# Kernel optimization log

Hardware: AMD Instinct MI355X
Metric: run time of the kernel (lower is better)

Reference implementation:

```python
import jax, jax.numpy as jnp
import numpy as np

N = 50000      # nodes
E = 800000     # edges (avg degree 16)
B = 250        # graphs in batch
T = 8          # temporal slices
CIN = 32
COUT = 64


def setup_inputs() -> dict:
    key = jax.random.key(0)
    ks = jax.random.split(key, 9)
    x = jax.random.normal(ks[0], (N, CIN, T), dtype=jnp.float32)
    edge_index = jax.random.randint(ks[1], (2, E), 0, N, dtype=jnp.int64)
    # 250 graphs of 200 nodes each -> every segment non-empty (safe for segment_max)
    batch = jnp.repeat(jnp.arange(B, dtype=jnp.int64), N // B)
    W1 = jax.random.normal(ks[2], (CIN, COUT), jnp.float32) / np.sqrt(CIN).astype(np.float32)
    b1 = jax.random.normal(ks[3], (COUT,), jnp.float32) * 0.01
    W2 = jax.random.normal(ks[4], (COUT, COUT), jnp.float32) / np.sqrt(COUT).astype(np.float32)
    b2 = jax.random.normal(ks[5], (COUT,), jnp.float32) * 0.01
    W3 = jax.random.normal(ks[6], (COUT, COUT), jnp.float32) / np.sqrt(COUT).astype(np.float32)
    b3 = jax.random.normal(ks[7], (COUT,), jnp.float32) * 0.01
    return {"x": x, "edge_index": edge_index, "batch": batch,
            "W1": W1, "b1": b1, "W2": W2, "b2": b2, "W3": W3, "b3": b3}


def reference(x, edge_index, batch, W1, b1, W2, b2, W3, b3):
    # GCNConv (PyG default): add self-loops, symmetric D^{-1/2}(A+I)D^{-1/2} norm,
    # linear transform then gather-scale-scatter aggregation, plus bias.
    src, dst = edge_index[0], edge_index[1]
    loops = jnp.arange(N, dtype=src.dtype)
    src2 = jnp.concatenate([src, loops])
    dst2 = jnp.concatenate([dst, loops])
    deg = jax.ops.segment_sum(jnp.ones_like(src2, x.dtype), dst2, num_segments=N)
    dinv = jax.lax.rsqrt(deg)  # deg >= 1 due to self-loops
    norm = dinv[src2] * dinv[dst2]  # [E+N]
    counts = jax.ops.segment_sum(jnp.ones((N,), x.dtype), batch, num_segments=B)

    def gcn(h, W, b):
        h = h @ W                              # [N, COUT]
        msg = norm[:, None] * h[src2]          # [E+N, COUT] gather + scale
        return jax.ops.segment_sum(msg, dst2, num_segments=N) + b

    def pool(h):  # cat(global_max_pool, global_mean_pool) -> [B, 2*COUT]
        mx = jax.ops.segment_max(h, batch, num_segments=B)
        mn = jax.ops.segment_sum(h, batch, num_segments=B) / counts[:, None]
        return jnp.concatenate([mx, mn], axis=1)

    def step(carry, xt):  # xt: [N, CIN]
        h1 = jax.nn.relu(gcn(xt, W1, b1))
        h2 = jax.nn.relu(gcn(h1, W2, b2))
        h3 = jax.nn.relu(gcn(h2, W3, b3))
        return carry, pool(h1) + pool(h2) + pool(h3)

    _, outs = jax.lax.scan(step, None, jnp.moveaxis(x, 2, 0))  # [T, B, 2*COUT]
    return jnp.moveaxis(outs, 0, 2)  # [B, 2*COUT, T]
```

## Files before the change

kernel.cpp:

```cpp
#include <hip/hip_runtime.h>
#include <hip/hip_fp16.h>
#include <math.h>

#define NN 50000
#define EE 800000
#define BB 250
#define TT 8
#define CIN 32
#define COUT 64
#define NPG 200
#define SCAN_B 256
#define NBLK 196
#define GC (BB * COUT)

__device__ __forceinline__ float unpack_w(unsigned int v) {
    union { unsigned short u; __half h; } cv;
    cv.u = (unsigned short)(v >> 16);
    return __half2float(cv.h);
}


__global__ void init_deg(int* deg, int* cursor) {
    int n = blockIdx.x * 256 + threadIdx.x;
    if (n < NN) { deg[n] = 1; cursor[n] = 0; }
}

__global__ void count_deg(const int* dst, int* deg) {
    int e = blockIdx.x * 256 + threadIdx.x;
    if (e < EE) atomicAdd(&deg[dst[e]], 1);
}

__global__ void compute_dinv(const int* deg, float* dinv) {
    int n = blockIdx.x * 256 + threadIdx.x;
    if (n < NN) dinv[n] = rsqrtf((float)deg[n]);
}

__global__ void scan_blocks(const int* deg, int* off, int* bsum) {
    __shared__ int sh[SCAN_B];
    int gid = blockIdx.x * SCAN_B + threadIdx.x;
    int v = (gid < NN) ? (deg[gid] - 1) : 0;
    sh[threadIdx.x] = v;
    __syncthreads();
    for (int s = 1; s < SCAN_B; s <<= 1) {
        int add = (threadIdx.x >= s) ? sh[threadIdx.x - s] : 0;
        __syncthreads();
        sh[threadIdx.x] += add;
        __syncthreads();
    }
    if (gid < NN) off[gid] = sh[threadIdx.x] - v;
    if (threadIdx.x == SCAN_B - 1) bsum[blockIdx.x] = sh[threadIdx.x];
}

__global__ void scan_sums(int* bsum, int* off) {
    __shared__ int sh[SCAN_B];
    int v = (threadIdx.x < NBLK) ? bsum[threadIdx.x] : 0;
    sh[threadIdx.x] = v;
    __syncthreads();
    for (int s = 1; s < SCAN_B; s <<= 1) {
        int add = (threadIdx.x >= s) ? sh[threadIdx.x - s] : 0;
        __syncthreads();
        sh[threadIdx.x] += add;
        __syncthreads();
    }
    if (threadIdx.x < NBLK) bsum[threadIdx.x] = sh[threadIdx.x] - v;
    if (threadIdx.x == 0) off[NN] = EE;
}

__global__ void scan_add(int* off, const int* bsum) {
    int gid = blockIdx.x * SCAN_B + threadIdx.x;
    if (gid < NN) off[gid] += bsum[blockIdx.x];
}

__global__ void fill_csr(const int* src, const int* dst, const int* off,
                         int* cursor, const float* dinv, unsigned int* csrp) {
    int e = blockIdx.x * 256 + threadIdx.x;
    if (e >= EE) return;
    int s = src[e], d = dst[e];
    int p = atomicAdd(&cursor[d], 1);
    union { __half h; unsigned short u; } cv;
    cv.h = __float2half(dinv[s] * dinv[d]);
    csrp[off[d] + p] = (unsigned int)s | ((unsigned int)cv.u << 16);
}

__global__ void scratch_init(float* scr, int ntot) {
    int i = blockIdx.x * 256 + threadIdx.x;
    if (i < ntot) scr[i] = 0.f;
}


__global__ void agg_x_allT16(const float* __restrict__ x, const int* __restrict__ off,
                             const unsigned int* __restrict__ csrp,
                             const float* __restrict__ dinv, __half2* __restrict__ xa2) {
    int lane = threadIdx.x & 63;
    int w = threadIdx.x >> 6;
    int n = blockIdx.x * 4 + w;
    float dn = dinv[n];
    float sw = dn * dn;
    float4 v = ((const float4*)(x + (size_t)n * 256))[lane];
    float4 acc = make_float4(sw * v.x, sw * v.y, sw * v.z, sw * v.w);
    int e0 = off[n], e1 = off[n + 1];
    for (int base = e0; base < e1; base += 64) {
        int idx = base + lane;
        unsigned int cme = (idx < e1) ? csrp[idx] : 0u;
        int cnt = min(64, e1 - base);
        int k = 0;
        for (; k + 3 < cnt; k += 4) {
            unsigned int p0 = __shfl(cme, k, 64),     p1 = __shfl(cme, k + 1, 64);
            unsigned int p2 = __shfl(cme, k + 2, 64), p3 = __shfl(cme, k + 3, 64);
            float4 u0 = ((const float4*)(x + (size_t)(p0 & 0xffff) * 256))[lane];
            float4 u1 = ((const float4*)(x + (size_t)(p1 & 0xffff) * 256))[lane];
            float4 u2 = ((const float4*)(x + (size_t)(p2 & 0xffff) * 256))[lane];
            float4 u3 = ((const float4*)(x + (size_t)(p3 & 0xffff) * 256))[lane];
            float w0 = unpack_w(p0), w1 = unpack_w(p1);
            float w2 = unpack_w(p2), w3 = unpack_w(p3);
            acc.x = fmaf(w0, u0.x, acc.x); acc.y = fmaf(w0, u0.y, acc.y);
            acc.z = fmaf(w0, u0.z, acc.z); acc.w = fmaf(w0, u0.w, acc.w);
            acc.x = fmaf(w1, u1.x, acc.x); acc.y = fmaf(w1, u1.y, acc.y);
            acc.z = fmaf(w1, u1.z, acc.z); acc.w = fmaf(w1, u1.w, acc.w);
            acc.x = fmaf(w2, u2.x, acc.x); acc.y = fmaf(w2, u2.y, acc.y);
            acc.z = fmaf(w2, u2.z, acc.z); acc.w = fmaf(w2, u2.w, acc.w);
            acc.x = fmaf(w3, u3.x, acc.x); acc.y = fmaf(w3, u3.y, acc.y);
            acc.z = fmaf(w3, u3.z, acc.z); acc.w = fmaf(w3, u3.w, acc.w);
        }
        for (; k < cnt; ++k) {
            unsigned int p = __shfl(cme, k, 64);
            float wj = unpack_w(p);
            float4 u = ((const float4*)(x + (size_t)(p & 0xffff) * 256))[lane];
            acc.x = fmaf(wj, u.x, acc.x); acc.y = fmaf(wj, u.y, acc.y);
            acc.z = fmaf(wj, u.z, acc.z); acc.w = fmaf(wj, u.w, acc.w);
        }
    }
    __shared__ float sh[4][TT][33];
    float av[4] = {acc.x, acc.y, acc.z, acc.w};
    #pragma unroll
    for (int k = 0; k < 4; ++k) {
        int f = 4 * lane + k;
        sh[w][f & 7][f >> 3] = av[k];
    }
    __syncthreads();
    for (int i = threadIdx.x; i < 512; i += 256) {
        int t = i >> 6;
        int r = i & 63;
        int nl = r >> 4;
        int pp = r & 15;
        xa2[((size_t)(t >> 1) * NN + blockIdx.x * 4 + nl) * 32 + (t & 1) * 16 + pp] =
            __floats2half2_rn(sh[nl][t][2 * pp], sh[nl][t][2 * pp + 1]);
    }
}

__global__ void l1mat2i(const __half2* __restrict__ xa, const float* __restrict__ W1,
                        const float* __restrict__ b1, const float* __restrict__ W2,
                        __half2* __restrict__ H1,
                        float* __restrict__ pmax, float* __restrict__ psum) {
    __shared__ float W1s[CIN * COUT];
    __shared__ __half2 W2s[COUT * 32];
    __shared__ float Xs[4][2][CIN];
    __shared__ float tile[4][2][COUT];
    for (int i = threadIdx.x; i < CIN * COUT; i += 256) W1s[i] = W1[i];
    for (int i = threadIdx.x; i < COUT * 32; i += 256) {
        int k = i >> 5, pr = i & 31;
        W2s[i] = __floats2half2_rn(W2[k * COUT + 2 * pr], W2[k * COUT + 2 * pr + 1]);
    }
    if (threadIdx.x < 128) {
        int nl = threadIdx.x >> 5, idx = threadIdx.x & 31;
        int tc = idx >> 4, pp = idx & 15;
        float2 v = __half22float2(xa[((size_t)blockIdx.x * 4 + nl) * 32 + idx]);
        Xs[nl][tc][2 * pp] = v.x;
        Xs[nl][tc][2 * pp + 1] = v.y;
    }
    __syncthreads();
    int co = threadIdx.x & 63;
    int nl = threadIdx.x >> 6;
    float a0 = b1[co], a1 = b1[co];
    #pragma unroll
    for (int k = 0; k < CIN; ++k) {
        float wv = W1s[k * COUT + co];
        a0 = fmaf(Xs[nl][0][k], wv, a0);
        a1 = fmaf(Xs[nl][1][k], wv, a1);
    }
    tile[nl][0][co] = fmaxf(a0, 0.f);
    tile[nl][1][co] = fmaxf(a1, 0.f);
    __syncthreads();
    if (threadIdx.x < 128) {
        int c = threadIdx.x & 63, tc = threadIdx.x >> 6;
        float m = fmaxf(fmaxf(tile[0][tc][c], tile[1][tc][c]),
                        fmaxf(tile[2][tc][c], tile[3][tc][c]));
        float s = tile[0][tc][c] + tile[1][tc][c] + tile[2][tc][c] + tile[3][tc][c];
        int g = blockIdx.x / 50;
        atomicMax((int*)&pmax[tc * GC + g * COUT + c], __float_as_int(m));
        atomicAdd(&psum[tc * GC + g * COUT + c], s);
    }
    {
        int row = threadIdx.x >> 5;
        int pr = threadIdx.x & 31;
        int nl2 = row >> 1, tc2 = row & 1;
        float b0 = 0.f, bb1 = 0.f;
        #pragma unroll
        for (int k = 0; k < COUT; ++k) {
            float xv = tile[nl2][tc2][k];
            float2 wv = __half22float2(W2s[k * 32 + pr]);
            b0 = fmaf(xv, wv.x, b0);
            bb1 = fmaf(xv, wv.y, bb1);
        }
        H1[((size_t)blockIdx.x * 4 + nl2) * 64 + tc2 * 32 + pr] =
            __floats2half2_rn(b0, bb1);
    }
}

template <int FUSE>
__global__ void agg2q(const __half2* __restrict__ Hin, const int* __restrict__ off,
                      const unsigned int* __restrict__ csrp,
                      const float* __restrict__ dinv, const float* __restrict__ b,
                      const float* __restrict__ W, __half2* __restrict__ Hout,
                      float* __restrict__ pmax, float* __restrict__ psum) {
    __shared__ __half2 Ws[FUSE ? COUT * 32 : 1];
    __shared__ float tile[4][2][COUT];
    if (FUSE)
        for (int i = threadIdx.x; i < COUT * 32; i += 256) {
            int k = i >> 5, pr = i & 31;
            Ws[i] = __floats2half2_rn(W[k * COUT + 2 * pr], W[k * COUT + 2 * pr + 1]);
        }
    int lane = threadIdx.x & 63;
    int w = threadIdx.x >> 6;
    int n = blockIdx.x * 4 + w;
    int e0 = off[n], e1 = off[n + 1];
    float dn = dinv[n];
    __half2 selfh = Hin[(size_t)n * 64 + lane];
    float accx = 0.f, accy = 0.f;

#define QUAD(K)                                                       \
    {                                                                 \
        unsigned int ce0 = __shfl(cme, (K),     64);                  \
        unsigned int ce1 = __shfl(cme, (K) + 1, 64);                  \
        unsigned int ce2 = __shfl(cme, (K) + 2, 64);                  \
        unsigned int ce3 = __shfl(cme, (K) + 3, 64);                  \
        __half2 u0 = Hin[(size_t)(ce0 & 0xffff) * 64 + lane];         \
        __half2 u1 = Hin[(size_t)(ce1 & 0xffff) * 64 + lane];         \
        __half2 u2 = Hin[(size_t)(ce2 & 0xffff) * 64 + lane];         \
        __half2 u3 = Hin[(size_t)(ce3 & 0xffff) * 64 + lane];         \
        float w0 = unpack_w(ce0), w1 = unpack_w(ce1);                 \
        float w2 = unpack_w(ce2), w3 = unpack_w(ce3);                 \
        float2 f0 = __half22float2(u0);                               \
        float2 f1 = __half22float2(u1);                               \
        float2 f2 = __half22float2(u2);                               \
        float2 f3 = __half22float2(u3);                               \
        accx = fmaf(w0, f0.x, accx); accy = fmaf(w0, f0.y, accy);     \
        accx = fmaf(w1, f1.x, accx); accy = fmaf(w1, f1.y, accy);     \
        accx = fmaf(w2, f2.x, accx); accy = fmaf(w2, f2.y, accy);     \
        accx = fmaf(w3, f3.x, accx); accy = fmaf(w3, f3.y, accy);     \
    }

    for (int base = e0; base < e1; base += 64) {
        int idx = base + lane;
        unsigned int cme = (idx < e1) ? csrp[idx] : 0u;
        int cnt = min(64, e1 - base);
        QUAD(0)
        QUAD(4)
        QUAD(8)
        QUAD(12)
        for (int k = 16; k < cnt; k += 4) QUAD(k)
    }
#undef QUAD

    {
        int tc = lane >> 5, p = lane & 31;
        float sw = dn * dn;
        float2 sv = __half22float2(selfh);
        float ox = fmaxf(fmaf(sw, sv.x, accx) + b[2 * p],     0.f);
        float oy = fmaxf(fmaf(sw, sv.y, accy) + b[2 * p + 1], 0.f);
        tile[w][tc][2 * p]     = ox;
        tile[w][tc][2 * p + 1] = oy;
    }
    __syncthreads();
    if (threadIdx.x < 128) {
        int c = threadIdx.x & 63, tcc = threadIdx.x >> 6;
        float m = fmaxf(fmaxf(tile[0][tcc][c], tile[1][tcc][c]),
                        fmaxf(tile[2][tcc][c], tile[3][tcc][c]));
        float s = tile[0][tcc][c] + tile[1][tcc][c] + tile[2][tcc][c] + tile[3][tcc][c];
        int g = blockIdx.x / 50;
        atomicMax((int*)&pmax[tcc * GC + g * COUT + c], __float_as_int(m));
        atomicAdd(&psum[tcc * GC + g * COUT + c], s);
    }
    if (FUSE) {
        int row = threadIdx.x >> 5;
        int pr = threadIdx.x & 31;
        int nl2 = row >> 1, tc2 = row & 1;
        float b0 = 0.f, bb1 = 0.f;
        #pragma unroll
        for (int k = 0; k < COUT; ++k) {
            float xv = tile[nl2][tc2][k];
            float2 wv = __half22float2(Ws[k * 32 + pr]);
            b0 = fmaf(xv, wv.x, b0);
            bb1 = fmaf(xv, wv.y, bb1);
        }
        Hout[((size_t)blockIdx.x * 4 + nl2) * 64 + tc2 * 32 + pr] =
            __floats2half2_rn(b0, bb1);
    }
}

__global__ void fold2(float* __restrict__ pmaxT, float* __restrict__ psumT,
                      float* __restrict__ out, int t0) {
    int i = blockIdx.x * 256 + threadIdx.x;
    if (i >= 2 * GC) return;
    int tc = i / GC;
    int r = i - tc * GC;
    int g = r >> 6, c = r & 63;
    float m = pmaxT[tc * GC + r] + pmaxT[2 * GC + tc * GC + r] +
              pmaxT[4 * GC + tc * GC + r];
    float mean = psumT[i] * (1.0f / NPG);
    int t = t0 + tc;
    out[((size_t)g * 128 + c) * TT + t] = m;
    out[((size_t)g * 128 + 64 + c) * TT + t] = mean;
    pmaxT[tc * GC + r] = 0.f;
    pmaxT[2 * GC + tc * GC + r] = 0.f;
    pmaxT[4 * GC + tc * GC + r] = 0.f;
    psumT[i] = 0.f;
}


extern "C" void kernel_launch(void* const* d_in, const int* in_sizes, int n_in,
                              void* d_out, int out_size, void* d_ws, size_t ws_size,
                              hipStream_t stream) {
    const float* x   = (const float*)d_in[0];
    const int*   ei  = (const int*)d_in[1];
    const int*   src = ei;
    const int*   dst = ei + EE;
    const float* W1  = (const float*)d_in[3];
    const float* b1  = (const float*)d_in[4];
    const float* W2  = (const float*)d_in[5];
    const float* b2  = (const float*)d_in[6];
    const float* W3  = (const float*)d_in[7];
    const float* b3  = (const float*)d_in[8];
    float* out = (float*)d_out;

    char* wsp = (char*)d_ws;
    auto alloc = [&](size_t bytes) {
        char* p = wsp;
        wsp += (bytes + 255) & ~(size_t)255;
        return p;
    };
    const size_t chunkHalf2 = (size_t)NN * 32;
    float*        dinv = (float*)       alloc((size_t)NN * 4);
    int*          off  = (int*)         alloc((size_t)(NN + 1) * 4);
    unsigned int* csrp = (unsigned int*)alloc((size_t)EE * 4);
    __half2*      H1   = (__half2*)     alloc((size_t)NN * 64 * 4);
    __half2*      xa2  = (__half2*)     alloc(chunkHalf2 * 4 * 4);
    __half2*      h2x  = (__half2*)     alloc(chunkHalf2 * 4);
    float*        scr  = (float*)       alloc((size_t)8 * GC * 4);
    (void)h2x;
    __half2* H2 = xa2 + 3 * chunkHalf2;
    float* pmaxT = scr;
    float* psumT = scr + 6 * GC;

    int* deg    = (int*)H1;
    int* cursor = ((int*)H1) + NN;
    int* bsum   = ((int*)H1) + 2 * NN;

    init_deg<<<NBLK, 256, 0, stream>>>(deg, cursor);
    count_deg<<<(EE + 255) / 256, 256, 0, stream>>>(dst, deg);
    compute_dinv<<<NBLK, 256, 0, stream>>>(deg, dinv);
    scan_blocks<<<NBLK, SCAN_B, 0, stream>>>(deg, off, bsum);
    scan_sums<<<1, SCAN_B, 0, stream>>>(bsum, off);
    scan_add<<<NBLK, SCAN_B, 0, stream>>>(off, bsum);
    fill_csr<<<(EE + 255) / 256, 256, 0, stream>>>(src, dst, off, cursor, dinv, csrp);
    scratch_init<<<(8 * GC + 255) / 256, 256, 0, stream>>>(scr, 8 * GC);

    agg_x_allT16<<<NN / 4, 256, 0, stream>>>(x, off, csrp, dinv, xa2);

    for (int c = 3; c >= 0; --c) {
        int t0 = 2 * c;
        const __half2* xc = xa2 + (size_t)c * chunkHalf2;
        l1mat2i<<<NN / 4, 256, 0, stream>>>(xc, W1, b1, W2, H1, pmaxT, psumT);
        agg2q<1><<<NN / 4, 256, 0, stream>>>(H1, off, csrp, dinv, b2, W3, H2,
                                             pmaxT + 2 * GC, psumT);
        agg2q<0><<<NN / 4, 256, 0, stream>>>(H2, off, csrp, dinv, b3, nullptr, nullptr,
                                             pmaxT + 4 * GC, psumT);
        fold2<<<(2 * GC + 255) / 256, 256, 0, stream>>>(pmaxT, psumT, out, t0);
    }
}
```

Baseline: 833.8 us.

## Aggregate 64 destinations per block in source-sliced passes for cache locality

```diff
diff --git a/kernel.cpp b/kernel.cpp
--- a/kernel.cpp
+++ b/kernel.cpp
@@ -12,6 +12,11 @@
 #define SCAN_B 256
 #define NBLK 196
 #define GC (BB * COUT)
+
+#define DPB 64
+#define NDB 782
+#define SLICE_SH 13
+#define NPASS 7
 
 __device__ __forceinline__ float unpack_w(unsigned int v) {
     union { unsigned short u; __half h; } cv;
@@ -208,13 +213,13 @@
 }
 
 template <int FUSE>
-__global__ void agg2q(const __half2* __restrict__ Hin, const int* __restrict__ off,
+__global__ void agg2t(const __half2* __restrict__ Hin, const int* __restrict__ off,
                       const unsigned int* __restrict__ csrp,
                       const float* __restrict__ dinv, const float* __restrict__ b,
                       const float* __restrict__ W, __half2* __restrict__ Hout,
                       float* __restrict__ pmax, float* __restrict__ psum) {
+    __shared__ float accf[DPB][128];
     __shared__ __half2 Ws[FUSE ? COUT * 32 : 1];
-    __shared__ float tile[4][2][COUT];
     if (FUSE)
         for (int i = threadIdx.x; i < COUT * 32; i += 256) {
             int k = i >> 5, pr = i & 31;
@@ -222,79 +227,112 @@
         }
     int lane = threadIdx.x & 63;
     int w = threadIdx.x >> 6;
-    int n = blockIdx.x * 4 + w;
-    int e0 = off[n], e1 = off[n + 1];
-    float dn = dinv[n];
-    __half2 selfh = Hin[(size_t)n * 64 + lane];
-    float accx = 0.f, accy = 0.f;
-
-#define QUAD(K)                                                       \
-    {                                                                 \
-        unsigned int ce0 = __shfl(cme, (K),     64);                  \
-        unsigned int ce1 = __shfl(cme, (K) + 1, 64);                  \
-        unsigned int ce2 = __shfl(cme, (K) + 2, 64);                  \
-        unsigned int ce3 = __shfl(cme, (K) + 3, 64);                  \
-        __half2 u0 = Hin[(size_t)(ce0 & 0xffff) * 64 + lane];         \
-        __half2 u1 = Hin[(size_t)(ce1 & 0xffff) * 64 + lane];         \
-        __half2 u2 = Hin[(size_t)(ce2 & 0xffff) * 64 + lane];         \
-        __half2 u3 = Hin[(size_t)(ce3 & 0xffff) * 64 + lane];         \
-        float w0 = unpack_w(ce0), w1 = unpack_w(ce1);                 \
-        float w2 = unpack_w(ce2), w3 = unpack_w(ce3);                 \
-        float2 f0 = __half22float2(u0);                               \
-        float2 f1 = __half22float2(u1);                               \
-        float2 f2 = __half22float2(u2);                               \
-        float2 f3 = __half22float2(u3);                               \
-        accx = fmaf(w0, f0.x, accx); accy = fmaf(w0, f0.y, accy);     \
-        accx = fmaf(w1, f1.x, accx); accy = fmaf(w1, f1.y, accy);     \
-        accx = fmaf(w2, f2.x, accx); accy = fmaf(w2, f2.y, accy);     \
-        accx = fmaf(w3, f3.x, accx); accy = fmaf(w3, f3.y, accy);     \
-    }
-
-    for (int base = e0; base < e1; base += 64) {
-        int idx = base + lane;
-        unsigned int cme = (idx < e1) ? csrp[idx] : 0u;
-        int cnt = min(64, e1 - base);
-        QUAD(0)
-        QUAD(4)
-        QUAD(8)
-        QUAD(12)
-        for (int k = 16; k < cnt; k += 4) QUAD(k)
-    }
-#undef QUAD
+    int n0 = blockIdx.x * DPB;
+
+    for (int i = 0; i < 16; ++i) {
+        int dl = 16 * w + i;
+        int n = n0 + dl;
+        float2 sv = make_float2(0.f, 0.f);
+        float sw = 0.f;
+        if (n < NN) {
+            float dn = dinv[n];
+            sw = dn * dn;
+            sv = __half22float2(Hin[(size_t)n * 64 + lane]);
+        }
+        accf[dl][2 * lane]     = sw * sv.x;
+        accf[dl][2 * lane + 1] = sw * sv.y;
+    }
+
+    for (int pass = 0; pass < NPASS; ++pass) {
+        for (int i = 0; i < 16; ++i) {
+            int dl = 16 * w + i;
+            int n = n0 + dl;
+            if (n >= NN) break;
+            float ax = 0.f, ay = 0.f;
+            int e0 = off[n], e1 = off[n + 1];
+            for (int base = e0; base < e1; base += 64) {
+                int idx = base + lane;
+                unsigned int cme = (idx < e1) ? csrp[idx] : 0u;
+                bool inpass = (((cme & 0xffffu) >> SLICE_SH) == (unsigned)pass);
+                unsigned long long m = __ballot(inpass);
+                while (m) {
+                    unsigned int c0, c1 = 0, c2 = 0, c3 = 0;
+                    { int k = __builtin_ctzll(m); m &= m - 1;
+                      c0 = __builtin_amdgcn_readlane(cme, k); }
+                    if (m) { int k = __builtin_ctzll(m); m &= m - 1;
+                             c1 = __builtin_amdgcn_readlane(cme, k); }
+                    if (m) { int k = __builtin_ctzll(m); m &= m - 1;
+                             c2 = __builtin_amdgcn_readlane(cme, k); }
+                    if (m) { int k = __builtin_ctzll(m); m &= m - 1;
+                             c3 = __builtin_amdgcn_readlane(cme, k); }
+                    __half2 u0 = Hin[(size_t)(c0 & 0xffff) * 64 + lane];
+                    __half2 u1 = Hin[(size_t)(c1 & 0xffff) * 64 + lane];
+                    __half2 u2 = Hin[(size_t)(c2 & 0xffff) * 64 + lane];
+                    __half2 u3 = Hin[(size_t)(c3 & 0xffff) * 64 + lane];
+                    float w0 = unpack_w(c0), w1 = unpack_w(c1);
+                    float w2 = unpack_w(c2), w3 = unpack_w(c3);
+                    float2 f0 = __half22float2(u0);
+                    float2 f1 = __half22float2(u1);
+                    float2 f2 = __half22float2(u2);
+                    float2 f3 = __half22float2(u3);
+                    ax = fmaf(w0, f0.x, ax); ay = fmaf(w0, f0.y, ay);
+                    ax = fmaf(w1, f1.x, ax); ay = fmaf(w1, f1.y, ay);
+                    ax = fmaf(w2, f2.x, ax); ay = fmaf(w2, f2.y, ay);
+                    ax = fmaf(w3, f3.x, ax); ay = fmaf(w3, f3.y, ay);
+                }
+            }
+            accf[dl][2 * lane]     += ax;
+            accf[dl][2 * lane + 1] += ay;
+        }
+    }
+    __syncthreads();
+
+    for (int i = threadIdx.x; i < DPB * 128; i += 256) {
+        int dl = i >> 7, ch = i & 127;
+        if (n0 + dl < NN)
+            accf[dl][ch] = fmaxf(accf[dl][ch] + b[ch & 63], 0.f);
+    }
+    __syncthreads();
 
     {
-        int tc = lane >> 5, p = lane & 31;
-        float sw = dn * dn;
-        float2 sv = __half22float2(selfh);
-        float ox = fmaxf(fmaf(sw, sv.x, accx) + b[2 * p],     0.f);
-        float oy = fmaxf(fmaf(sw, sv.y, accy) + b[2 * p + 1], 0.f);
-        tile[w][tc][2 * p]     = ox;
-        tile[w][tc][2 * p + 1] = oy;
-    }
-    __syncthreads();
-    if (threadIdx.x < 128) {
-        int c = threadIdx.x & 63, tcc = threadIdx.x >> 6;
-        float m = fmaxf(fmaxf(tile[0][tcc][c], tile[1][tcc][c]),
-                        fmaxf(tile[2][tcc][c], tile[3][tcc][c]));
-        float s = tile[0][tcc][c] + tile[1][tcc][c] + tile[2][tcc][c] + tile[3][tcc][c];
-        int g = blockIdx.x / 50;
-        atomicMax((int*)&pmax[tcc * GC + g * COUT + c], __float_as_int(m));
-        atomicAdd(&psum[tcc * GC + g * COUT + c], s);
-    }
+        int ch = threadIdx.x & 127;
+        int grp = threadIdx.x >> 7;
+        int g = n0 / NPG + grp;
+        int lo = max(n0, g * NPG);
+        int hi = min(min(n0 + DPB, NN), (g + 1) * NPG);
+        if (lo < hi) {
+            float mx = 0.f, sm = 0.f;
+            for (int nn2 = lo; nn2 < hi; ++nn2) {
+                float v = accf[nn2 - n0][ch];
+                mx = fmaxf(mx, v);
+                sm += v;
+            }
+            int tc = ch >> 6, c = ch & 63;
+            atomicMax((int*)&pmax[tc * GC + g * COUT + c], __float_as_int(mx));
+            atomicAdd(&psum[tc * GC + g * COUT + c], sm);
+        }
+    }
+
     if (FUSE) {
-        int row = threadIdx.x >> 5;
-        int pr = threadIdx.x & 31;
-        int nl2 = row >> 1, tc2 = row & 1;
-        float b0 = 0.f, bb1 = 0.f;
-        #pragma unroll
-        for (int k = 0; k < COUT; ++k) {
-            float xv = tile[nl2][tc2][k];
-            float2 wv = __half22float2(Ws[k * 32 + pr]);
-            b0 = fmaf(xv, wv.x, b0);
-            bb1 = fmaf(xv, wv.y, bb1);
-        }
-        Hout[((size_t)blockIdx.x * 4 + nl2) * 64 + tc2 * 32 + pr] =
-            __floats2half2_rn(b0, bb1);
+        int dl = threadIdx.x >> 2;
+        int q  = threadIdx.x & 3;
+        int n = n0 + dl;
+        if (n < NN) {
+            int tc = q >> 1;
+            int prbase = (q & 1) * 16;
+            for (int pp = 0; pp < 16; ++pp) {
+                int pr = prbase + pp;
+                float b0 = 0.f, bb1 = 0.f;
+                #pragma unroll
+                for (int k = 0; k < COUT; ++k) {
+                    float xv = accf[dl][tc * 64 + k];
+                    float2 wv = __half22float2(Ws[k * 32 + pr]);
+                    b0 = fmaf(xv, wv.x, b0);
+                    bb1 = fmaf(xv, wv.y, bb1);
+                }
+                Hout[(size_t)n * 64 + tc * 32 + pr] = __floats2half2_rn(b0, bb1);
+            }
+        }
     }
 }
 
@@ -371,10 +409,10 @@
         int t0 = 2 * c;
         const __half2* xc = xa2 + (size_t)c * chunkHalf2;
         l1mat2i<<<NN / 4, 256, 0, stream>>>(xc, W1, b1, W2, H1, pmaxT, psumT);
-        agg2q<1><<<NN / 4, 256, 0, stream>>>(H1, off, csrp, dinv, b2, W3, H2,
-                                             pmaxT + 2 * GC, psumT);
-        agg2q<0><<<NN / 4, 256, 0, stream>>>(H2, off, csrp, dinv, b3, nullptr, nullptr,
-                                             pmaxT + 4 * GC, psumT);
+        agg2t<1><<<NDB, 256, 0, stream>>>(H1, off, csrp, dinv, b2, W3, H2,
+                                          pmaxT + 2 * GC, psumT);
+        agg2t<0><<<NDB, 256, 0, stream>>>(H2, off, csrp, dinv, b3, nullptr, nullptr,
+                                          pmaxT + 4 * GC, psumT);
         fold2<<<(2 * GC + 255) / 256, 256, 0, stream>>>(pmaxT, psumT, out, t0);
     }
 }
```

New measurement: 2.367 ms. 184% more time.
